# Optimization experiments

Measured on AMD Instinct MI355X. Metric: run time of the kernel, lower is better.

Reference implementation:

```python
import jax, jax.numpy as jnp
import numpy as np

EMBED_DIM = 1024
NUM_HEADS = 16
HEAD_DIM = EMBED_DIM // NUM_HEADS


def setup_inputs() -> dict:
    key = jax.random.key(0)
    ks = jax.random.split(key, 5)
    B, S, E = 2, 2048, EMBED_DIM
    # xavier-uniform-ish scale for square linear weights
    lim = float(np.sqrt(6.0 / (E + E)))
    x = jax.random.normal(ks[0], (B, S, E), dtype=jnp.float32)
    Wq = jax.random.uniform(ks[1], (E, E), jnp.float32, -lim, lim)
    Wk = jax.random.uniform(ks[2], (E, E), jnp.float32, -lim, lim)
    Wv = jax.random.uniform(ks[3], (E, E), jnp.float32, -lim, lim)
    Wo = jax.random.uniform(ks[4], (E, E), jnp.float32, -lim, lim)
    z = jnp.zeros((E,), jnp.float32)
    return {"x": x, "Wq": Wq, "bq": z, "Wk": Wk, "bk": z,
            "Wv": Wv, "bv": z, "Wo": Wo, "bo": z}


def reference(x, Wq, bq, Wk, bk, Wv, bv, Wo, bo):
    B, S, E = x.shape
    H, Dh = NUM_HEADS, HEAD_DIM
    # Linear projections (torch Linear: y = x @ W.T + b)
    q = (x @ Wq.T + bq).reshape(B, S, H, Dh).transpose(0, 2, 1, 3)  # [B,H,S,Dh]
    k = (x @ Wk.T + bk).reshape(B, S, H, Dh).transpose(0, 2, 1, 3)
    v = (x @ Wv.T + bv).reshape(B, S, H, Dh).transpose(0, 2, 1, 3)
    # NOTE: module scales by 1/head_dim (not 1/sqrt(head_dim)) — faithful.
    logits = jnp.einsum('bhqd,bhkd->bhqk', q, k) / Dh  # [B,H,S,S]
    attn = jax.nn.softmax(logits, axis=-1)
    vals = jnp.einsum('bhqk,bhkd->bhqd', attn, v)      # [B,H,S,Dh]
    vals = vals.transpose(0, 2, 1, 3).reshape(B, S, E)
    out = vals @ Wo.T + bo
    return out
```

## Files before the change

### kernel.cpp

```cpp
#include <hip/hip_runtime.h>
#include <hip/hip_bf16.h>

#define EDIM 1024
#define NH   16
#define DH   64
#define BB   2
#define SS   2048
#define MM   (BB*SS)

typedef unsigned short u16;
typedef __attribute__((ext_vector_type(4))) float f32x4;
typedef __attribute__((ext_vector_type(8))) short s16x8;

__device__ __forceinline__ u16 f2bf(float x) {
    __hip_bfloat16 b = __float2bfloat16(x);
    return *(u16*)&b;
}

__device__ __forceinline__ void gload16(const void* g, void* l) {
    __builtin_amdgcn_global_load_lds(
        (const __attribute__((address_space(1))) unsigned int*)g,
        (__attribute__((address_space(3))) unsigned int*)l, 16, 0, 0);
}

__global__ __launch_bounds__(256) void convert_all(const float* __restrict__ x,
                                                   const float* __restrict__ Wq,
                                                   const float* __restrict__ Wk,
                                                   const float* __restrict__ Wv,
                                                   const float* __restrict__ Wo,
                                                   u16* __restrict__ xh,
                                                   u16* __restrict__ wqkv,
                                                   u16* __restrict__ woh)
{
    const int i = blockIdx.x * 256 + threadIdx.x;
    const float* src; ushort4* dst; int off;
    if (i < 1048576)      { src = x;  dst = (ushort4*)xh;   off = i; }
    else if (i < 1310720) { src = Wq; dst = (ushort4*)wqkv; off = i - 1048576; }
    else if (i < 1572864) { src = Wk; dst = (ushort4*)wqkv; off = i - 1310720 + 262144; }
    else if (i < 1835008) { src = Wv; dst = (ushort4*)wqkv; off = i - 1572864 + 524288; }
    else                  { src = Wo; dst = (ushort4*)woh;  off = i - 1835008; }
    const int so = (i < 1048576) ? i
                 : (i < 1310720) ? (i - 1048576)
                 : (i < 1572864) ? (i - 1310720)
                 : (i < 1835008) ? (i - 1572864) : (i - 1835008);
    const float4 v = ((const float4*)src)[so];
    ushort4 h;
    h.x = f2bf(v.x); h.y = f2bf(v.y); h.z = f2bf(v.z); h.w = f2bf(v.w);
    dst[off] = h;
}

__global__ __launch_bounds__(256) void gemm_qkv(const u16* __restrict__ A,
                                                const u16* __restrict__ B,
                                                const float* __restrict__ bq,
                                                const float* __restrict__ bk,
                                                const float* __restrict__ bv,
                                                u16* __restrict__ qb,
                                                u16* __restrict__ kb,
                                                u16* __restrict__ vT)
{
    __shared__ __align__(16) u16 As[128][32];
    __shared__ __align__(16) u16 Bs[128][32];

    const int tid  = threadIdx.x;
    const int lane = tid & 63, wid = tid >> 6;
    const int wm = wid >> 1, wn = wid & 1;
    const int swz   = (blockIdx.x & 7) * 96 + (blockIdx.x >> 3);
    const int m0 = (swz & 31) * 128;
    const int n0 = (swz >> 5) * 128;

    f32x4 acc[4][4];
    #pragma unroll
    for (int i = 0; i < 4; ++i)
        #pragma unroll
        for (int j = 0; j < 4; ++j) acc[i][j] = f32x4{0.f, 0.f, 0.f, 0.f};

    const int lrow0 = tid >> 2;
    const int lcol  = (tid & 3) * 8;

    for (int k0 = 0; k0 < 1024; k0 += 32) {
        __syncthreads();
        gload16(A + (size_t)(m0 + lrow0)      * 1024 + k0 + lcol, (char*)As + wid * 1024);
        gload16(A + (size_t)(m0 + 64 + lrow0) * 1024 + k0 + lcol, (char*)As + 4096 + wid * 1024);
        gload16(B + (size_t)(n0 + lrow0)      * 1024 + k0 + lcol, (char*)Bs + wid * 1024);
        gload16(B + (size_t)(n0 + 64 + lrow0) * 1024 + k0 + lcol, (char*)Bs + 4096 + wid * 1024);
        __syncthreads();

        s16x8 af[4], bf[4];
        #pragma unroll
        for (int i = 0; i < 4; ++i) {
            af[i] = *(const s16x8*)&As[wm * 64 + i * 16 + (lane & 15)][(lane >> 4) * 8];
            bf[i] = *(const s16x8*)&Bs[wn * 64 + i * 16 + (lane & 15)][(lane >> 4) * 8];
        }
        #pragma unroll
        for (int i = 0; i < 4; ++i)
            #pragma unroll
            for (int j = 0; j < 4; ++j)
                acc[i][j] = __builtin_amdgcn_mfma_f32_16x16x32_bf16(af[i], bf[j], acc[i][j], 0, 0, 0);
    }

    #pragma unroll
    for (int i = 0; i < 4; ++i) {
        const int mbase = m0 + wm * 64 + i * 16 + ((lane >> 4) * 4);
        #pragma unroll
        for (int j = 0; j < 4; ++j) {
            const int n = n0 + wn * 64 + j * 16 + (lane & 15);
            const float bias = (n < 1024) ? bq[n] : (n < 2048) ? bk[n - 1024] : bv[n - 2048];
            #pragma unroll
            for (int r = 0; r < 4; ++r) {
                const int m = mbase + r;
                const int b_ = m >> 11, s_ = m & 2047;
                const u16 val = f2bf(acc[i][j][r] + bias);
                if (n < 1024) {
                    const int h_ = n >> 6, d_ = n & 63;
                    qb[((size_t)(b_ * NH + h_) * SS + s_) * DH + d_] = val;
                } else if (n < 2048) {
                    const int h_ = (n >> 6) & 15, d_ = n & 63;
                    kb[((size_t)(b_ * NH + h_) * SS + s_) * DH + d_] = val;
                } else {
                    const int hd = n - 2048;
                    vT[((size_t)(b_ * EDIM) + hd) * SS + s_] = val;
                }
            }
        }
    }
}

__global__ __launch_bounds__(256) void gemm_out(const u16* __restrict__ A,
                                                const u16* __restrict__ B,
                                                const float* __restrict__ bo,
                                                float* __restrict__ out)
{
    __shared__ __align__(16) u16 As[64][32];
    __shared__ __align__(16) u16 Bs[128][32];

    const int tid  = threadIdx.x;
    const int lane = tid & 63, wid = tid >> 6;
    const int wm = wid >> 1, wn = wid & 1;
    const int swz = (blockIdx.x & 7) * 64 + (blockIdx.x >> 3);
    const int m0 = (swz & 63) * 64;
    const int n0 = (swz >> 6) * 128;

    f32x4 acc[2][4];
    #pragma unroll
    for (int i = 0; i < 2; ++i)
        #pragma unroll
        for (int j = 0; j < 4; ++j) acc[i][j] = f32x4{0.f, 0.f, 0.f, 0.f};

    const int lrow0 = tid >> 2;
    const int lcol  = (tid & 3) * 8;

    for (int k0 = 0; k0 < 1024; k0 += 32) {
        __syncthreads();
        gload16(A + (size_t)(m0 + lrow0)      * 1024 + k0 + lcol, (char*)As + wid * 1024);
        gload16(B + (size_t)(n0 + lrow0)      * 1024 + k0 + lcol, (char*)Bs + wid * 1024);
        gload16(B + (size_t)(n0 + 64 + lrow0) * 1024 + k0 + lcol, (char*)Bs + 4096 + wid * 1024);
        __syncthreads();

        s16x8 af[2], bf[4];
        #pragma unroll
        for (int i = 0; i < 2; ++i)
            af[i] = *(const s16x8*)&As[wm * 32 + i * 16 + (lane & 15)][(lane >> 4) * 8];
        #pragma unroll
        for (int j = 0; j < 4; ++j)
            bf[j] = *(const s16x8*)&Bs[wn * 64 + j * 16 + (lane & 15)][(lane >> 4) * 8];
        #pragma unroll
        for (int i = 0; i < 2; ++i)
            #pragma unroll
            for (int j = 0; j < 4; ++j)
                acc[i][j] = __builtin_amdgcn_mfma_f32_16x16x32_bf16(af[i], bf[j], acc[i][j], 0, 0, 0);
    }

    #pragma unroll
    for (int i = 0; i < 2; ++i) {
        const int mbase = m0 + wm * 32 + i * 16 + ((lane >> 4) * 4);
        #pragma unroll
        for (int j = 0; j < 4; ++j) {
            const int n = n0 + wn * 64 + j * 16 + (lane & 15);
            #pragma unroll
            for (int r = 0; r < 4; ++r)
                out[(size_t)(mbase + r) * EDIM + n] = acc[i][j][r] + bo[n];
        }
    }
}

__global__ __launch_bounds__(256) void attn_mfma(const u16* __restrict__ q,
                                                 const u16* __restrict__ k,
                                                 const u16* __restrict__ vT,
                                                 u16* __restrict__ valsh)
{
    __shared__ __align__(16) u16 kt[128][64];
    __shared__ __align__(16) u16 vt[64][128];
    __shared__ __align__(16) u16 pt[128][128];

    const int tid = threadIdx.x, lane = tid & 63, wid = tid >> 6;
    const int swz = (blockIdx.x & 7) * 64 + (blockIdx.x >> 3);
    const int bh = swz >> 4, qt = swz & 15;
    const int b = bh >> 4, h = bh & 15;
    const int qr0 = wid * 32;

    const char* qbase = (const char*)(q + ((size_t)bh * SS + qt * 128) * DH);
    #pragma unroll
    for (int i = 0; i < 4; ++i) {
        const int flat = i * 256 + tid;
        const int row = flat >> 3, u = flat & 7;
        gload16(qbase + row * 128 + ((u ^ (row & 7)) << 4),
                (char*)kt + (i * 256 + wid * 64) * 16);
    }
    __syncthreads();
    s16x8 qf[2][2];
    #pragma unroll
    for (int mi = 0; mi < 2; ++mi)
        #pragma unroll
        for (int kk = 0; kk < 2; ++kk) {
            const int row = qr0 + mi * 16 + (lane & 15);
            const int u   = (kk * 4 + (lane >> 4)) ^ (row & 7);
            qf[mi][kk] = *(const s16x8*)((const char*)kt + row * 128 + u * 16);
        }
    __syncthreads();

    f32x4 acc_o[2][4];
    #pragma unroll
    for (int mi = 0; mi < 2; ++mi)
        #pragma unroll
        for (int ni = 0; ni < 4; ++ni) acc_o[mi][ni] = f32x4{0.f, 0.f, 0.f, 0.f};
    float rs[2][4] = {};

    const char* kbh = (const char*)(k + (size_t)bh * SS * DH);
    const char* vbh = (const char*)(vT + ((size_t)b * EDIM + h * DH) * SS);

    #pragma unroll 1
    for (int c0 = 0; c0 < SS; c0 += 128) {
        #pragma unroll
        for (int i = 0; i < 4; ++i) {
            const int flat = i * 256 + tid;
            const int row = flat >> 3, u = flat & 7;
            gload16(kbh + (size_t)(c0 + row) * 128 + ((u ^ (row & 7)) << 4),
                    (char*)kt + (i * 256 + wid * 64) * 16);
        }
        #pragma unroll
        for (int i = 0; i < 4; ++i) {
            const int flat = i * 256 + tid;
            const int row = flat >> 4, u = flat & 15;
            gload16(vbh + (size_t)row * (SS * 2) + (size_t)c0 * 2 + ((u ^ (row & 15)) << 4),
                    (char*)vt + (i * 256 + wid * 64) * 16);
        }
        __syncthreads();

        #pragma unroll
        for (int mi = 0; mi < 2; ++mi) {
            f32x4 sc[8];
            #pragma unroll
            for (int ni = 0; ni < 8; ++ni) sc[ni] = f32x4{0.f, 0.f, 0.f, 0.f};
            #pragma unroll
            for (int ni = 0; ni < 8; ++ni)
                #pragma unroll
                for (int kk = 0; kk < 2; ++kk) {
                    const int row = ni * 16 + (lane & 15);
                    const int u   = (kk * 4 + (lane >> 4)) ^ (row & 7);
                    const s16x8 kf = *(const s16x8*)((const char*)kt + row * 128 + u * 16);
                    sc[ni] = __builtin_amdgcn_mfma_f32_16x16x32_bf16(qf[mi][kk], kf, sc[ni], 0, 0, 0);
                }

            float lrs[4] = {0.f, 0.f, 0.f, 0.f};
            #pragma unroll
            for (int ni = 0; ni < 8; ++ni)
                #pragma unroll
                for (int r = 0; r < 4; ++r) {
                    const float p = exp2f(sc[ni][r] * 0.02254211f);
                    sc[ni][r] = p;
                    lrs[r] += p;
                }
            #pragma unroll
            for (int mask = 1; mask < 16; mask <<= 1)
                #pragma unroll
                for (int r = 0; r < 4; ++r) lrs[r] += __shfl_xor(lrs[r], mask, 64);
            #pragma unroll
            for (int r = 0; r < 4; ++r) rs[mi][r] += lrs[r];

            #pragma unroll
            for (int ni = 0; ni < 8; ++ni) {
                const int col = ni * 16 + (lane & 15);
                #pragma unroll
                for (int r = 0; r < 4; ++r) {
                    const int row = qr0 + mi * 16 + (lane >> 4) * 4 + r;
                    const int u   = (col >> 3) ^ (row & 15);
                    *(u16*)((char*)pt + row * 256 + u * 16 + (col & 7) * 2) = f2bf(sc[ni][r]);
                }
            }
        }
        __syncthreads();

        #pragma unroll
        for (int kk = 0; kk < 4; ++kk) {
            s16x8 pf[2], vf[4];
            #pragma unroll
            for (int mi = 0; mi < 2; ++mi) {
                const int row = qr0 + mi * 16 + (lane & 15);
                const int u   = (kk * 4 + (lane >> 4)) ^ (row & 15);
                pf[mi] = *(const s16x8*)((const char*)pt + row * 256 + u * 16);
            }
            #pragma unroll
            for (int ni = 0; ni < 4; ++ni) {
                const int row = ni * 16 + (lane & 15);
                const int u   = (kk * 4 + (lane >> 4)) ^ (row & 15);
                vf[ni] = *(const s16x8*)((const char*)vt + row * 256 + u * 16);
            }
            #pragma unroll
            for (int mi = 0; mi < 2; ++mi)
                #pragma unroll
                for (int ni = 0; ni < 4; ++ni)
                    acc_o[mi][ni] = __builtin_amdgcn_mfma_f32_16x16x32_bf16(pf[mi], vf[ni], acc_o[mi][ni], 0, 0, 0);
        }
        __syncthreads();
    }

    #pragma unroll
    for (int mi = 0; mi < 2; ++mi) {
        float inv[4];
        #pragma unroll
        for (int r = 0; r < 4; ++r) inv[r] = 1.f / rs[mi][r];
        #pragma unroll
        for (int ni = 0; ni < 4; ++ni)
            #pragma unroll
            for (int r = 0; r < 4; ++r) {
                const int srow = qt * 128 + qr0 + mi * 16 + (lane >> 4) * 4 + r;
                const int col  = h * 64 + ni * 16 + (lane & 15);
                valsh[(size_t)(b * SS + srow) * EDIM + col] = f2bf(acc_o[mi][ni][r] * inv[r]);
            }
    }
}

extern "C" void kernel_launch(void* const* d_in, const int* in_sizes, int n_in,
                              void* d_out, int out_size, void* d_ws, size_t ws_size,
                              hipStream_t stream)
{
    const float* x  = (const float*)d_in[0];
    const float* Wq = (const float*)d_in[1];
    const float* bq = (const float*)d_in[2];
    const float* Wk = (const float*)d_in[3];
    const float* bk = (const float*)d_in[4];
    const float* Wv = (const float*)d_in[5];
    const float* bv = (const float*)d_in[6];
    const float* Wo = (const float*)d_in[7];
    const float* bo = (const float*)d_in[8];
    float* out = (float*)d_out;

    u16* W = (u16*)d_ws;
    const size_t M1 = 1024 * 1024;
    u16* xh    = W;
    u16* wqkv  = W + 4  * M1;
    u16* woh   = W + 7  * M1;
    u16* qbuf  = W + 8  * M1;
    u16* kbuf  = W + 12 * M1;
    u16* vbufT = W + 16 * M1;
    u16* valsh = W + 20 * M1;

    convert_all<<<dim3(8192), 256, 0, stream>>>(x, Wq, Wk, Wv, Wo, xh, wqkv, woh);

    gemm_qkv<<<dim3(768), 256, 0, stream>>>(xh, wqkv, bq, bk, bv, qbuf, kbuf, vbufT);

    attn_mfma<<<dim3(BB * NH * (SS / 128)), 256, 0, stream>>>(qbuf, kbuf, vbufT, valsh);

    gemm_out<<<dim3(512), 256, 0, stream>>>(valsh, woh, bo, out);
}
```

Before: 240.2 us.

## Keep attention probabilities in registers using 32x32 MFMA and permlane swaps

Rewrites the attention inner loop to compute transposed scores (K·Q^T) with 32x32x16 bf16 MFMA, so each lane holds a column of probabilities. These are packed to bf16 with v_cvt_pk_bf16_f32 and rearranged with v_permlane32_swap to feed the PV MFMA directly, removing the P shared-memory round trip, one barrier per chunk and the per-chunk row-sum shuffles. Q fragments are loaded straight from global, s_setprio brackets the MFMA bursts, and the QKV GEMM epilogue branches once per block instead of per element. This relies on gfx950-specific instructions and on the register layout mapping being correct.

```diff
diff --git a/kernel.cpp b/kernel.cpp
--- a/kernel.cpp
+++ b/kernel.cpp
@@ -9,12 +9,22 @@
 #define MM   (BB*SS)
 
 typedef unsigned short u16;
-typedef __attribute__((ext_vector_type(4))) float f32x4;
-typedef __attribute__((ext_vector_type(8))) short s16x8;
+typedef unsigned int   u32;
+typedef __attribute__((ext_vector_type(4)))  float f32x4;
+typedef __attribute__((ext_vector_type(16))) float f32x16;
+typedef __attribute__((ext_vector_type(8)))  short s16x8;
 
 __device__ __forceinline__ u16 f2bf(float x) {
     __hip_bfloat16 b = __float2bfloat16(x);
     return *(u16*)&b;
+}
+__device__ __forceinline__ u32 cvtpk(float lo, float hi_) {
+    u32 r;
+    asm("v_cvt_pk_bf16_f32 %0, %1, %2" : "=v"(r) : "v"(lo), "v"(hi_));
+    return r;
+}
+__device__ __forceinline__ void swap32(u32& a, u32& b) {
+    asm("v_permlane32_swap_b32 %0, %1" : "+v"(a), "+v"(b));
 }
 
 __device__ __forceinline__ void gload16(const void* g, void* l) {
@@ -98,27 +108,54 @@
                 acc[i][j] = __builtin_amdgcn_mfma_f32_16x16x32_bf16(af[i], bf[j], acc[i][j], 0, 0, 0);
     }
 
-    #pragma unroll
-    for (int i = 0; i < 4; ++i) {
-        const int mbase = m0 + wm * 64 + i * 16 + ((lane >> 4) * 4);
-        #pragma unroll
-        for (int j = 0; j < 4; ++j) {
-            const int n = n0 + wn * 64 + j * 16 + (lane & 15);
-            const float bias = (n < 1024) ? bq[n] : (n < 2048) ? bk[n - 1024] : bv[n - 2048];
-            #pragma unroll
-            for (int r = 0; r < 4; ++r) {
-                const int m = mbase + r;
-                const int b_ = m >> 11, s_ = m & 2047;
-                const u16 val = f2bf(acc[i][j][r] + bias);
-                if (n < 1024) {
-                    const int h_ = n >> 6, d_ = n & 63;
-                    qb[((size_t)(b_ * NH + h_) * SS + s_) * DH + d_] = val;
-                } else if (n < 2048) {
-                    const int h_ = (n >> 6) & 15, d_ = n & 63;
-                    kb[((size_t)(b_ * NH + h_) * SS + s_) * DH + d_] = val;
-                } else {
-                    const int hd = n - 2048;
-                    vT[((size_t)(b_ * EDIM) + hd) * SS + s_] = val;
+    if (n0 < 1024) {
+        #pragma unroll
+        for (int i = 0; i < 4; ++i) {
+            const int mbase = m0 + wm * 64 + i * 16 + ((lane >> 4) * 4);
+            #pragma unroll
+            for (int j = 0; j < 4; ++j) {
+                const int n = n0 + wn * 64 + j * 16 + (lane & 15);
+                const float bias = bq[n];
+                const int h_ = n >> 6, d_ = n & 63;
+                #pragma unroll
+                for (int r = 0; r < 4; ++r) {
+                    const int m = mbase + r;
+                    const int b_ = m >> 11, s_ = m & 2047;
+                    qb[((size_t)(b_ * NH + h_) * SS + s_) * DH + d_] = f2bf(acc[i][j][r] + bias);
+                }
+            }
+        }
+    } else if (n0 < 2048) {
+        #pragma unroll
+        for (int i = 0; i < 4; ++i) {
+            const int mbase = m0 + wm * 64 + i * 16 + ((lane >> 4) * 4);
+            #pragma unroll
+            for (int j = 0; j < 4; ++j) {
+                const int n = n0 + wn * 64 + j * 16 + (lane & 15);
+                const float bias = bk[n - 1024];
+                const int h_ = (n >> 6) & 15, d_ = n & 63;
+                #pragma unroll
+                for (int r = 0; r < 4; ++r) {
+                    const int m = mbase + r;
+                    const int b_ = m >> 11, s_ = m & 2047;
+                    kb[((size_t)(b_ * NH + h_) * SS + s_) * DH + d_] = f2bf(acc[i][j][r] + bias);
+                }
+            }
+        }
+    } else {
+        #pragma unroll
+        for (int i = 0; i < 4; ++i) {
+            const int mbase = m0 + wm * 64 + i * 16 + ((lane >> 4) * 4);
+            #pragma unroll
+            for (int j = 0; j < 4; ++j) {
+                const int n = n0 + wn * 64 + j * 16 + (lane & 15);
+                const float bias = bv[n - 2048];
+                const int hd = n - 2048;
+                #pragma unroll
+                for (int r = 0; r < 4; ++r) {
+                    const int m = mbase + r;
+                    const int b_ = m >> 11, s_ = m & 2047;
+                    vT[((size_t)(b_ * EDIM) + hd) * SS + s_] = f2bf(acc[i][j][r] + bias);
                 }
             }
         }
@@ -190,40 +227,24 @@
 {
     __shared__ __align__(16) u16 kt[128][64];
     __shared__ __align__(16) u16 vt[64][128];
-    __shared__ __align__(16) u16 pt[128][128];
 
     const int tid = threadIdx.x, lane = tid & 63, wid = tid >> 6;
+    const int lq = lane & 31, hi = lane >> 5;
     const int swz = (blockIdx.x & 7) * 64 + (blockIdx.x >> 3);
     const int bh = swz >> 4, qt = swz & 15;
     const int b = bh >> 4, h = bh & 15;
-    const int qr0 = wid * 32;
-
-    const char* qbase = (const char*)(q + ((size_t)bh * SS + qt * 128) * DH);
-    #pragma unroll
-    for (int i = 0; i < 4; ++i) {
-        const int flat = i * 256 + tid;
-        const int row = flat >> 3, u = flat & 7;
-        gload16(qbase + row * 128 + ((u ^ (row & 7)) << 4),
-                (char*)kt + (i * 256 + wid * 64) * 16);
-    }
-    __syncthreads();
-    s16x8 qf[2][2];
-    #pragma unroll
-    for (int mi = 0; mi < 2; ++mi)
-        #pragma unroll
-        for (int kk = 0; kk < 2; ++kk) {
-            const int row = qr0 + mi * 16 + (lane & 15);
-            const int u   = (kk * 4 + (lane >> 4)) ^ (row & 7);
-            qf[mi][kk] = *(const s16x8*)((const char*)kt + row * 128 + u * 16);
-        }
-    __syncthreads();
-
-    f32x4 acc_o[2][4];
-    #pragma unroll
-    for (int mi = 0; mi < 2; ++mi)
-        #pragma unroll
-        for (int ni = 0; ni < 4; ++ni) acc_o[mi][ni] = f32x4{0.f, 0.f, 0.f, 0.f};
-    float rs[2][4] = {};
+
+    const u16* qg = q + ((size_t)bh * SS + qt * 128 + wid * 32 + lq) * DH + hi * 8;
+    s16x8 qf[4];
+    #pragma unroll
+    for (int ks = 0; ks < 4; ++ks) qf[ks] = *(const s16x8*)(qg + ks * 16);
+
+    f32x16 acc_o[2];
+    #pragma unroll
+    for (int db = 0; db < 2; ++db)
+        #pragma unroll
+        for (int r = 0; r < 16; ++r) acc_o[db][r] = 0.f;
+    float rs = 0.f;
 
     const char* kbh = (const char*)(k + (size_t)bh * SS * DH);
     const char* vbh = (const char*)(vT + ((size_t)b * EDIM + h * DH) * SS);
@@ -247,87 +268,71 @@
         __syncthreads();
 
         #pragma unroll
-        for (int mi = 0; mi < 2; ++mi) {
-            f32x4 sc[8];
-            #pragma unroll
-            for (int ni = 0; ni < 8; ++ni) sc[ni] = f32x4{0.f, 0.f, 0.f, 0.f};
-            #pragma unroll
-            for (int ni = 0; ni < 8; ++ni)
+        for (int kb = 0; kb < 4; ++kb) {
+            f32x16 sc;
+            #pragma unroll
+            for (int r = 0; r < 16; ++r) sc[r] = 0.f;
+            const int krow = kb * 32 + lq;
+            __builtin_amdgcn_s_setprio(1);
+            #pragma unroll
+            for (int ks = 0; ks < 4; ++ks) {
+                const int u = (ks * 2 + hi) ^ (krow & 7);
+                const s16x8 kf = *(const s16x8*)((const char*)kt + krow * 128 + u * 16);
+                sc = __builtin_amdgcn_mfma_f32_32x32x16_bf16(kf, qf[ks], sc, 0, 0, 0);
+            }
+            __builtin_amdgcn_s_setprio(0);
+
+            #pragma unroll
+            for (int r = 0; r < 16; ++r) {
+                sc[r] = __builtin_amdgcn_exp2f(sc[r] * 0.0225421209f);
+                rs += sc[r];
+            }
+
+            u32 w0 = cvtpk(sc[0],  sc[1]),  w1 = cvtpk(sc[2],  sc[3]);
+            u32 w2 = cvtpk(sc[4],  sc[5]),  w3 = cvtpk(sc[6],  sc[7]);
+            u32 w4 = cvtpk(sc[8],  sc[9]),  w5 = cvtpk(sc[10], sc[11]);
+            u32 w6 = cvtpk(sc[12], sc[13]), w7 = cvtpk(sc[14], sc[15]);
+            swap32(w0, w2);
+            swap32(w1, w3);
+            swap32(w4, w6);
+            swap32(w5, w7);
+            union { u32 w[4]; s16x8 v; } pa0, pa1;
+            pa0.w[0] = w0; pa0.w[1] = w1; pa0.w[2] = w2; pa0.w[3] = w3;
+            pa1.w[0] = w4; pa1.w[1] = w5; pa1.w[2] = w6; pa1.w[3] = w7;
+
+            __builtin_amdgcn_s_setprio(1);
+            #pragma unroll
+            for (int t = 0; t < 2; ++t) {
+                const s16x8 pat = t ? pa1.v : pa0.v;
+                const int kst = kb * 2 + t;
                 #pragma unroll
-                for (int kk = 0; kk < 2; ++kk) {
-                    const int row = ni * 16 + (lane & 15);
-                    const int u   = (kk * 4 + (lane >> 4)) ^ (row & 7);
-                    const s16x8 kf = *(const s16x8*)((const char*)kt + row * 128 + u * 16);
-                    sc[ni] = __builtin_amdgcn_mfma_f32_16x16x32_bf16(qf[mi][kk], kf, sc[ni], 0, 0, 0);
+                for (int db = 0; db < 2; ++db) {
+                    const int vrow = db * 32 + lq;
+                    const int u = (kst * 2 + hi) ^ (vrow & 15);
+                    const s16x8 vf = *(const s16x8*)((const char*)vt + vrow * 256 + u * 16);
+                    acc_o[db] = __builtin_amdgcn_mfma_f32_32x32x16_bf16(pat, vf, acc_o[db], 0, 0, 0);
                 }
-
-            float lrs[4] = {0.f, 0.f, 0.f, 0.f};
-            #pragma unroll
-            for (int ni = 0; ni < 8; ++ni)
-                #pragma unroll
-                for (int r = 0; r < 4; ++r) {
-                    const float p = exp2f(sc[ni][r] * 0.02254211f);
-                    sc[ni][r] = p;
-                    lrs[r] += p;
-                }
-            #pragma unroll
-            for (int mask = 1; mask < 16; mask <<= 1)
-                #pragma unroll
-                for (int r = 0; r < 4; ++r) lrs[r] += __shfl_xor(lrs[r], mask, 64);
-            #pragma unroll
-            for (int r = 0; r < 4; ++r) rs[mi][r] += lrs[r];
-
-            #pragma unroll
-            for (int ni = 0; ni < 8; ++ni) {
-                const int col = ni * 16 + (lane & 15);
-                #pragma unroll
-                for (int r = 0; r < 4; ++r) {
-                    const int row = qr0 + mi * 16 + (lane >> 4) * 4 + r;
-                    const int u   = (col >> 3) ^ (row & 15);
-                    *(u16*)((char*)pt + row * 256 + u * 16 + (col & 7) * 2) = f2bf(sc[ni][r]);
-                }
-            }
-        }
-        __syncthreads();
-
-        #pragma unroll
-        for (int kk = 0; kk < 4; ++kk) {
-            s16x8 pf[2], vf[4];
-            #pragma unroll
-            for (int mi = 0; mi < 2; ++mi) {
-                const int row = qr0 + mi * 16 + (lane & 15);
-                const int u   = (kk * 4 + (lane >> 4)) ^ (row & 15);
-                pf[mi] = *(const s16x8*)((const char*)pt + row * 256 + u * 16);
-            }
-            #pragma unroll
-            for (int ni = 0; ni < 4; ++ni) {
-                const int row = ni * 16 + (lane & 15);
-                const int u   = (kk * 4 + (lane >> 4)) ^ (row & 15);
-                vf[ni] = *(const s16x8*)((const char*)vt + row * 256 + u * 16);
-            }
-            #pragma unroll
-            for (int mi = 0; mi < 2; ++mi)
-                #pragma unroll
-                for (int ni = 0; ni < 4; ++ni)
-                    acc_o[mi][ni] = __builtin_amdgcn_mfma_f32_16x16x32_bf16(pf[mi], vf[ni], acc_o[mi][ni], 0, 0, 0);
-        }
-        __syncthreads();
-    }
-
-    #pragma unroll
-    for (int mi = 0; mi < 2; ++mi) {
-        float inv[4];
-        #pragma unroll
-        for (int r = 0; r < 4; ++r) inv[r] = 1.f / rs[mi][r];
-        #pragma unroll
-        for (int ni = 0; ni < 4; ++ni)
-            #pragma unroll
-            for (int r = 0; r < 4; ++r) {
-                const int srow = qt * 128 + qr0 + mi * 16 + (lane >> 4) * 4 + r;
-                const int col  = h * 64 + ni * 16 + (lane & 15);
-                valsh[(size_t)(b * SS + srow) * EDIM + col] = f2bf(acc_o[mi][ni][r] * inv[r]);
-            }
-    }
+            }
+            __builtin_amdgcn_s_setprio(0);
+        }
+        __syncthreads();
+    }
+
+    const float rsf = rs + __shfl_xor(rs, 32, 64);
+    const float inv = 1.f / rsf;
+    float iv[16];
+    #pragma unroll
+    for (int r = 0; r < 16; ++r)
+        iv[r] = __shfl(inv, (r & 3) + 8 * (r >> 2) + 4 * hi, 64);
+
+    #pragma unroll
+    for (int db = 0; db < 2; ++db)
+        #pragma unroll
+        for (int r = 0; r < 16; ++r) {
+            const int srow = qt * 128 + wid * 32 + (r & 3) + 8 * (r >> 2) + 4 * hi;
+            const int col  = h * 64 + db * 32 + lq;
+            valsh[(size_t)(b * SS + srow) * EDIM + col] = f2bf(acc_o[db][r] * iv[r]);
+        }
 }
 
 extern "C" void kernel_launch(void* const* d_in, const int* in_sizes, int n_in,
```

After: 205.2 us. -14.6%, faster.
